# Kernel optimization log

Hardware: AMD Instinct MI355X
Metric: run time of the kernel (lower is better)

Reference implementation:

```python
import jax, jax.numpy as jnp
import numpy as np

B, S, D_MODEL, N_HEAD, D_HEAD = 4, 2048, 512, 8, 64


def setup_inputs() -> dict:
    key = jax.random.key(0)
    ks = jax.random.split(key, 12)
    s = 0.02
    Q = jax.random.normal(ks[0], (B, S, D_MODEL), jnp.float32)
    K = jax.random.normal(ks[1], (B, S, D_MODEL), jnp.float32)
    V = jax.random.normal(ks[2], (B, S, D_MODEL), jnp.float32)
    # causal 0/1 mask, 1 = masked-out (scores get -1e9*mask)
    causal = jnp.triu(jnp.ones((S, S), jnp.float32), k=1)
    attn_mask = jnp.broadcast_to(causal, (B, S, S))
    Wq = jax.random.normal(ks[3], (D_MODEL, N_HEAD * D_HEAD), jnp.float32) * s
    bq = jnp.zeros((N_HEAD * D_HEAD,), jnp.float32)
    Wk = jax.random.normal(ks[4], (D_MODEL, N_HEAD * D_HEAD), jnp.float32) * s
    bk = jnp.zeros((N_HEAD * D_HEAD,), jnp.float32)
    Wv = jax.random.normal(ks[5], (D_MODEL, N_HEAD * D_HEAD), jnp.float32) * s
    bv = jnp.zeros((N_HEAD * D_HEAD,), jnp.float32)
    Wo = jax.random.normal(ks[6], (N_HEAD * D_HEAD, D_MODEL), jnp.float32) * s
    bo = jnp.zeros((D_MODEL,), jnp.float32)
    return {"Q": Q, "K": K, "V": V, "attn_mask": attn_mask,
            "Wq": Wq, "bq": bq, "Wk": Wk, "bk": bk,
            "Wv": Wv, "bv": bv, "Wo": Wo, "bo": bo}


def reference(Q, K, V, attn_mask, Wq, bq, Wk, bk, Wv, bv, Wo, bo):
    # project and split heads: [B,S,D] -> [B,H,S,Dh]
    def heads(x, W, b):
        return (x @ W + b).reshape(B, S, N_HEAD, D_HEAD).transpose(0, 2, 1, 3)

    Qh, Kh, Vh = heads(Q, Wq, bq), heads(K, Wk, bk), heads(V, Wv, bv)
    scale = jnp.sqrt(jnp.asarray(D_HEAD, jnp.float32))
    scores = jnp.einsum('bhqd,bhkd->bhqk', Qh, Kh) / scale  # [B,H,S,S]
    scores = scores - 1e9 * attn_mask[:, None, :, :]
    probs = jax.nn.softmax(scores, axis=-1)
    out = jnp.einsum('bhqk,bhkd->bhqd', probs, Vh)
    out = out.transpose(0, 2, 1, 3).reshape(B, S, N_HEAD * D_HEAD)
    return out @ Wo + bo
```

## Files before the change

kernel.cpp:

```cpp
#include <hip/hip_runtime.h>
#include <hip/hip_bf16.h>
#include <cstdint>
#include <cstddef>

#define B_DIM   4
#define S_DIM   2048
#define DMODEL  512
#define N_HEAD  8
#define D_HEAD  64
#define M_TOT   (B_DIM*S_DIM)

typedef __attribute__((ext_vector_type(8))) short bf16x8;
typedef __attribute__((ext_vector_type(4))) float f32x4;
typedef __attribute__((ext_vector_type(4))) unsigned short us4;
typedef __attribute__((ext_vector_type(2))) unsigned int u32x2;
typedef __attribute__((ext_vector_type(4))) unsigned int u32x4;

static __device__ __forceinline__ unsigned short f2bf(float x) {
  unsigned int u = __float_as_uint(x);
  unsigned int r = (u + 0x7fffu + ((u >> 16) & 1u)) >> 16;
  return (unsigned short)r;
}

static __device__ __forceinline__ unsigned int cvtpk(float lo, float hi) {
  unsigned int r;
  asm("v_cvt_pk_bf16_f32 %0, %1, %2" : "=v"(r) : "v"(lo), "v"(hi));
  return r;
}

static __device__ __forceinline__ void gl2lds16(const unsigned short* g, unsigned short* l) {
  __builtin_amdgcn_global_load_lds(
      (const __attribute__((address_space(1))) void*)g,
      (__attribute__((address_space(3))) void*)l, 16, 0, 0);
}
static __device__ __forceinline__ void gl2lds16f(const float* g, float* l) {
  __builtin_amdgcn_global_load_lds(
      (const __attribute__((address_space(1))) void*)g,
      (__attribute__((address_space(3))) void*)l, 16, 0, 0);
}

__global__ __launch_bounds__(256) void wprep_kernel(
    const float* __restrict__ wq, const float* __restrict__ wk,
    const float* __restrict__ wv, const float* __restrict__ wo,
    unsigned short* __restrict__ out)
{
  __shared__ float T[64][65];
  const int w = blockIdx.x >> 6, tile = blockIdx.x & 63;
  const float* W = (w==0)? wq : (w==1)? wk : (w==2)? wv : wo;
  unsigned short* O = out + (size_t)w*DMODEL*DMODEL;
  const int k0 = (tile>>3)*64, n0 = (tile&7)*64;
  const int tid = threadIdx.x;
  #pragma unroll
  for (int i=0;i<16;i++){
    int flat = tid + i*256; int r = flat>>6, c = flat&63;
    T[r][c] = W[(size_t)(k0+r)*DMODEL + n0 + c];
  }
  __syncthreads();
  #pragma unroll
  for (int i=0;i<16;i++){
    int flat = tid + i*256; int r = flat>>6, c = flat&63;
    O[(size_t)(n0+r)*DMODEL + k0 + c] = f2bf(T[c][r]);
  }
}

__global__ __launch_bounds__(256) void proj_kernel(
    const float* __restrict__ Qf, const float* __restrict__ Kf,
    const float* __restrict__ Vf, const unsigned short* __restrict__ Wtr,
    const float* __restrict__ bq, const float* __restrict__ bk, const float* __restrict__ bv,
    unsigned short* __restrict__ Qh, unsigned short* __restrict__ Kh, unsigned short* __restrict__ Vht)
{
  __shared__ __align__(16) float          Af[2][128*32];
  __shared__ __align__(16) unsigned short Bt[2][128*32];
  const int mode = blockIdx.z;
  const float* A = (mode==0)? Qf : (mode==1)? Kf : Vf;
  const unsigned short* Wt = Wtr + (size_t)mode*DMODEL*DMODEL;
  const float* bias = (mode==0)? bq : (mode==1)? bk : bv;
  const int tid = threadIdx.x, wave = tid>>6, lane = tid&63;
  const int g = lane>>4, ln = lane&15;
  const int mB = blockIdx.y*128, nB = blockIdx.x*128;
  const int mw = (wave>>1)*64,  nw = (wave&1)*64;
  const int lrowA = lane>>3, suF = ((lane&7) ^ (lane>>3))*4;
  const int srow = lane>>2, scolE = (lane&3)*8;
  const int cA = 2*wave, cB = 2*wave+1;

  #define STG(buf, k0_)                                                        \
    do {                                                                       \
      _Pragma("unroll")                                                        \
      for (int q=0;q<4;q++)                                                    \
        gl2lds16f(A + (size_t)(mB + (wave*4+q)*8 + lrowA)*DMODEL + (k0_) + suF,\
                  &Af[buf][(wave*4+q)*256]);                                   \
      gl2lds16(Wt + (size_t)(nB + cA*16 + srow)*DMODEL + (k0_) + scolE, &Bt[buf][cA*512]); \
      gl2lds16(Wt + (size_t)(nB + cB*16 + srow)*DMODEL + (k0_) + scolE, &Bt[buf][cB*512]); \
    } while (0)

  f32x4 acc[4][4];
  #pragma unroll
  for (int i=0;i<4;i++)
    #pragma unroll
    for (int jj=0;jj<4;jj++) acc[i][jj]=(f32x4){0.f,0.f,0.f,0.f};

  STG(0, 0);
  __syncthreads();
  for (int s=0; s<16; ++s){
    const int cur = s&1;
    if (s+1 < 16) STG(cur^1, (s+1)*32);
    bf16x8 a[4], bb[4];
    #pragma unroll
    for (int rf=0;rf<4;rf++){
      const int row = mw + rf*16 + ln;
      const int u0 = (2*g)   ^ (ln&7);
      const int u1 = (2*g+1) ^ (ln&7);
      f32x4 x0 = *(const f32x4*)&Af[cur][row*32 + u0*4];
      f32x4 x1 = *(const f32x4*)&Af[cur][row*32 + u1*4];
      union { u32x4 u; bf16x8 b; } t;
      t.u[0] = cvtpk(x0[0], x0[1]);
      t.u[1] = cvtpk(x0[2], x0[3]);
      t.u[2] = cvtpk(x1[0], x1[1]);
      t.u[3] = cvtpk(x1[2], x1[3]);
      a[rf] = t.b;
    }
    #pragma unroll
    for (int cf=0;cf<4;cf++) bb[cf] = *(const bf16x8*)(&Bt[cur][(nw + cf*16 + ln)*32 + g*8]);
    __builtin_amdgcn_s_setprio(1);
    #pragma unroll
    for (int rf=0;rf<4;rf++)
      #pragma unroll
      for (int cf=0;cf<4;cf++)
        acc[rf][cf] = __builtin_amdgcn_mfma_f32_16x16x32_bf16(a[rf], bb[cf], acc[rf][cf], 0,0,0);
    __builtin_amdgcn_s_setprio(0);
    __syncthreads();
  }
  #undef STG

  const int m0 = mB + mw, n0 = nB + nw;
  float bvv[4];
  #pragma unroll
  for (int cf=0;cf<4;cf++) bvv[cf] = bias[n0 + cf*16 + ln];
  const float QSC = 0.18033688011112042f;

  if (mode <= 1) {
    unsigned short* O = (mode==0)? Qh : Kh;
    const float sc = (mode==0)? QSC : 1.0f;
    #pragma unroll
    for (int rf=0;rf<4;rf++){
      int m = m0 + rf*16 + 4*g;
      int b2 = m >> 11, sdx = m & (S_DIM-1);
      #pragma unroll
      for (int cf=0;cf<4;cf++){
        int n = n0 + cf*16 + ln;
        int h = n >> 6, d = n & 63;
        size_t base = ((size_t)(b2*N_HEAD + h)*S_DIM + sdx)*D_HEAD + d;
        #pragma unroll
        for (int r=0;r<4;r++)
          O[base + (size_t)r*D_HEAD] = f2bf((acc[rf][cf][r] + bvv[cf]) * sc);
      }
    }
  } else {
    #pragma unroll
    for (int rf=0;rf<4;rf++){
      int m = m0 + rf*16 + 4*g;
      int b2 = m >> 11, sdx = m & (S_DIM-1);
      #pragma unroll
      for (int cf=0;cf<4;cf++){
        int n = n0 + cf*16 + ln;
        int h = n >> 6, d = n & 63;
        us4 pk;
        #pragma unroll
        for (int r=0;r<4;r++) pk[r] = f2bf(acc[rf][cf][r] + bvv[cf]);
        *(us4*)&Vht[((size_t)(b2*N_HEAD + h)*D_HEAD + d)*S_DIM + sdx] = pk;
      }
    }
  }
}

__global__ __launch_bounds__(512,4) void attn_kernel(
    const unsigned short* __restrict__ Qh, const unsigned short* __restrict__ Kh,
    const unsigned short* __restrict__ Vht, unsigned short* __restrict__ AO)
{
  __shared__ __align__(16) unsigned short Kt[2][64*64];
  __shared__ __align__(16) unsigned short Vt[2][64*64];
  __shared__ __align__(16) unsigned short Plds[8][16][72];

  const int tid = threadIdx.x, wave = tid>>6, lane = tid&63;
  const int g = lane>>4, ln = lane&15;
  const int j = blockIdx.x;
  const int xcd = j & 7, rest = j >> 3;
  const int bh = xcd*4 + (rest & 3);
  const int t  = 15 - (rest >> 2);
  const int qrow0 = t*128 + wave*16;
  const int q_i = qrow0 + ln;
  const int nit = 2*t + 2;
  const int b = bh >> 3, h = bh & 7;

  const unsigned short* Qp = Qh  + (size_t)bh*S_DIM*D_HEAD;
  const unsigned short* Kp = Kh  + (size_t)bh*S_DIM*D_HEAD;
  const unsigned short* Vp = Vht + (size_t)bh*D_HEAD*S_DIM;

  const int lrow = lane >> 3;
  const int scol = (((lane & 7) ^ lrow) << 3);
  const int swz  = (lane & 7) << 3;
  const unsigned short* kg = Kp + (size_t)(wave*8 + lrow)*64 + scol;
  const unsigned short* vg = Vp + (size_t)(wave*8 + lrow)*S_DIM + scol;

  #define STG_KV(buf, k0_)                                   \
    do {                                                     \
      gl2lds16(kg + (size_t)(k0_)*64, &Kt[buf][wave*512]);   \
      gl2lds16(vg + (k0_),            &Vt[buf][wave*512]);   \
    } while (0)

  bf16x8 qf0 = *(const bf16x8*)(Qp + (size_t)(qrow0+ln)*D_HEAD + 8*g);
  bf16x8 qf1 = *(const bf16x8*)(Qp + (size_t)(qrow0+ln)*D_HEAD + 32 + 8*g);

  f32x4 o[4];
  #pragma unroll
  for (int cc=0;cc<4;cc++) o[cc] = (f32x4){0.f,0.f,0.f,0.f};
  float lsum = 0.f;

  STG_KV(0, 0);
  __syncthreads();

  for (int it = 0; it < nit; ++it) {
    const int cur = it & 1;
    if (it + 1 < nit) STG_KV(cur^1, (it+1)*64);
    const unsigned short* Kc = Kt[cur];
    const unsigned short* Vc = Vt[cur];

    f32x4 s[4];
    __builtin_amdgcn_s_setprio(1);
    #pragma unroll
    for (int i=0;i<4;i++){
      const int r = i*16 + ln;
      bf16x8 ka0 = *(const bf16x8*)(Kc + r*64 + ((g*8) ^ swz));
      bf16x8 ka1 = *(const bf16x8*)(Kc + r*64 + ((32 + g*8) ^ swz));
      f32x4 z = (f32x4){0.f,0.f,0.f,0.f};
      z = __builtin_amdgcn_mfma_f32_16x16x32_bf16(ka0, qf0, z, 0,0,0);
      z = __builtin_amdgcn_mfma_f32_16x16x32_bf16(ka1, qf1, z, 0,0,0);
      s[i] = z;
    }
    __builtin_amdgcn_s_setprio(0);
    const int k0 = it*64;
    if (k0 + 63 > q_i - ln) {
      #pragma unroll
      for (int i=0;i<4;i++)
        #pragma unroll
        for (int r=0;r<4;r++)
          if (k0 + i*16 + 4*g + r > q_i) s[i][r] = -1e30f;
    }
    float p[4][4];
    #pragma unroll
    for (int i=0;i<4;i++)
      #pragma unroll
      for (int r=0;r<4;r++){
        float e = __builtin_amdgcn_exp2f(s[i][r]);
        p[i][r] = e; lsum += e;
      }
    #pragma unroll
    for (int i=0;i<4;i++){
      u32x2 pk2;
      pk2[0] = cvtpk(p[i][0], p[i][1]);
      pk2[1] = cvtpk(p[i][2], p[i][3]);
      *(u32x2*)&Plds[wave][ln][i*16 + 4*g] = pk2;
    }
    bf16x8 pa0 = *(const bf16x8*)&Plds[wave][ln][8*g];
    bf16x8 pa1 = *(const bf16x8*)&Plds[wave][ln][32 + 8*g];
    __builtin_amdgcn_s_setprio(1);
    #pragma unroll
    for (int cc=0;cc<4;cc++){
      const int r = cc*16 + ln;
      bf16x8 vb0 = *(const bf16x8*)(Vc + r*64 + ((g*8) ^ swz));
      bf16x8 vb1 = *(const bf16x8*)(Vc + r*64 + ((32 + g*8) ^ swz));
      o[cc] = __builtin_amdgcn_mfma_f32_16x16x32_bf16(pa0, vb0, o[cc], 0,0,0);
      o[cc] = __builtin_amdgcn_mfma_f32_16x16x32_bf16(pa1, vb1, o[cc], 0,0,0);
    }
    __builtin_amdgcn_s_setprio(0);
    __syncthreads();
  }
  #undef STG_KV

  float lt = lsum;
  lt += __shfl_xor(lt, 16, 64);
  lt += __shfl_xor(lt, 32, 64);
  #pragma unroll
  for (int r=0;r<4;r++){
    float lq  = __shfl(lt, 4*g + r, 64);
    float inv = 1.0f / lq;
    int srow2 = qrow0 + 4*g + r;
    size_t base = ((size_t)b*S_DIM + srow2)*DMODEL + h*D_HEAD;
    #pragma unroll
    for (int cc=0;cc<4;cc++)
      AO[base + cc*16 + ln] = f2bf(o[cc][r]*inv);
  }
}

__global__ __launch_bounds__(256) void outproj_kernel(
    const unsigned short* __restrict__ AO, const unsigned short* __restrict__ Wt,
    const float* __restrict__ bo, float* __restrict__ Out)
{
  __shared__ __align__(16) unsigned short At[2][128*32];
  __shared__ __align__(16) unsigned short Bt[2][128*32];
  const int tid = threadIdx.x, wave = tid>>6, lane = tid&63;
  const int g = lane>>4, ln = lane&15;
  const int mB = blockIdx.y*128, nB = blockIdx.x*128;
  const int mw = (wave>>1)*64,  nw = (wave&1)*64;
  const int srow = lane>>2, scolE = (lane&3)*8;
  const int cA = 2*wave, cB = 2*wave+1;

  #define STG_G(buf, k0_)                                                      \
    do {                                                                       \
      gl2lds16(AO + (size_t)(mB + cA*16 + srow)*DMODEL + (k0_) + scolE, &At[buf][cA*512]); \
      gl2lds16(AO + (size_t)(mB + cB*16 + srow)*DMODEL + (k0_) + scolE, &At[buf][cB*512]); \
      gl2lds16(Wt + (size_t)(nB + cA*16 + srow)*DMODEL + (k0_) + scolE, &Bt[buf][cA*512]); \
      gl2lds16(Wt + (size_t)(nB + cB*16 + srow)*DMODEL + (k0_) + scolE, &Bt[buf][cB*512]); \
    } while (0)

  f32x4 acc[4][4];
  #pragma unroll
  for (int i=0;i<4;i++)
    #pragma unroll
    for (int jj=0;jj<4;jj++) acc[i][jj]=(f32x4){0.f,0.f,0.f,0.f};

  STG_G(0, 0);
  __syncthreads();
  for (int s=0; s<16; ++s){
    const int cur = s&1;
    if (s+1 < 16) STG_G(cur^1, (s+1)*32);
    bf16x8 a[4], bb[4];
    #pragma unroll
    for (int rf=0;rf<4;rf++) a[rf]  = *(const bf16x8*)(&At[cur][(mw + rf*16 + ln)*32 + g*8]);
    #pragma unroll
    for (int cf=0;cf<4;cf++) bb[cf] = *(const bf16x8*)(&Bt[cur][(nw + cf*16 + ln)*32 + g*8]);
    __builtin_amdgcn_s_setprio(1);
    #pragma unroll
    for (int rf=0;rf<4;rf++)
      #pragma unroll
      for (int cf=0;cf<4;cf++)
        acc[rf][cf] = __builtin_amdgcn_mfma_f32_16x16x32_bf16(a[rf], bb[cf], acc[rf][cf], 0,0,0);
    __builtin_amdgcn_s_setprio(0);
    __syncthreads();
  }
  #undef STG_G

  const int m0 = mB + mw, n0 = nB + nw;
  float bvv[4];
  #pragma unroll
  for (int cf=0;cf<4;cf++) bvv[cf] = bo[n0 + cf*16 + ln];
  #pragma unroll
  for (int rf=0;rf<4;rf++){
    #pragma unroll
    for (int cf=0;cf<4;cf++){
      int n = n0 + cf*16 + ln;
      #pragma unroll
      for (int r=0;r<4;r++){
        int m = m0 + rf*16 + 4*g + r;
        Out[(size_t)m*DMODEL + n] = acc[rf][cf][r] + bvv[cf];
      }
    }
  }
}

extern "C" void kernel_launch(void* const* d_in, const int* in_sizes, int n_in,
                              void* d_out, int out_size, void* d_ws, size_t ws_size,
                              hipStream_t stream)
{
  const float* Q  = (const float*)d_in[0];
  const float* K  = (const float*)d_in[1];
  const float* V  = (const float*)d_in[2];
  const float* Wq = (const float*)d_in[4];
  const float* bq = (const float*)d_in[5];
  const float* Wk = (const float*)d_in[6];
  const float* bk = (const float*)d_in[7];
  const float* Wv = (const float*)d_in[8];
  const float* bv = (const float*)d_in[9];
  const float* Wo = (const float*)d_in[10];
  const float* bo = (const float*)d_in[11];

  unsigned short* ws = (unsigned short*)d_ws;
  const size_t TEN = (size_t)M_TOT * DMODEL;
  unsigned short* Wtr = ws;
  unsigned short* Qh  = Wtr + (size_t)4*DMODEL*DMODEL;
  unsigned short* Kh  = Qh + TEN;
  unsigned short* Vht = Kh + TEN;
  unsigned short* AO  = Vht + TEN;

  wprep_kernel  <<<dim3(256),    256, 0, stream>>>(Wq,Wk,Wv,Wo,Wtr);
  proj_kernel   <<<dim3(4,64,3), 256, 0, stream>>>(Q,K,V,Wtr,bq,bk,bv,Qh,Kh,Vht);
  attn_kernel   <<<dim3(512),    512, 0, stream>>>(Qh,Kh,Vht,AO);
  outproj_kernel<<<dim3(4,64),   256, 0, stream>>>(AO, Wtr + (size_t)3*DMODEL*DMODEL, bo, (float*)d_out);
}
```

Measured before the change: 226.9 us.

## Fuse all four stages into one cooperative persistent kernel with grid syncs

Replaces the four separate launches (weight prep, QKV projection, attention, output projection) with a single cooperative kernel of 256 blocks of 512 threads. Grid-wide syncs separate the stages, and one 64 KB LDS arena is reused by every stage. Projection tiles grow to 128x256 per block, and each attention block handles two causal q-tiles (t and 15-t) to balance work. The aim is to remove launch gaps and tail effects between kernels. The cost is fewer blocks in flight (256 versus 512 or 768 before), idle blocks during the projection and output stages, and grid.sync overhead.

Measured after the change: 571.5 us. 2.52x slower.

```diff
diff --git a/kernel.cpp b/kernel.cpp
--- a/kernel.cpp
+++ b/kernel.cpp
@@ -1,7 +1,10 @@
 #include <hip/hip_runtime.h>
+#include <hip/hip_cooperative_groups.h>
 #include <hip/hip_bf16.h>
 #include <cstdint>
 #include <cstddef>
+
+namespace cg = cooperative_groups;
 
 #define B_DIM   4
 #define S_DIM   2048
@@ -21,13 +24,11 @@
   unsigned int r = (u + 0x7fffu + ((u >> 16) & 1u)) >> 16;
   return (unsigned short)r;
 }
-
 static __device__ __forceinline__ unsigned int cvtpk(float lo, float hi) {
   unsigned int r;
   asm("v_cvt_pk_bf16_f32 %0, %1, %2" : "=v"(r) : "v"(lo), "v"(hi));
   return r;
 }
-
 static __device__ __forceinline__ void gl2lds16(const unsigned short* g, unsigned short* l) {
   __builtin_amdgcn_global_load_lds(
       (const __attribute__((address_space(1))) void*)g,
@@ -39,320 +40,320 @@
       (__attribute__((address_space(3))) void*)l, 16, 0, 0);
 }
 
-__global__ __launch_bounds__(256) void wprep_kernel(
-    const float* __restrict__ wq, const float* __restrict__ wk,
-    const float* __restrict__ wv, const float* __restrict__ wo,
-    unsigned short* __restrict__ out)
+__global__ __launch_bounds__(512,2) void fused_kernel(
+    const float* __restrict__ Q, const float* __restrict__ K, const float* __restrict__ V,
+    const float* __restrict__ Wq, const float* __restrict__ bq,
+    const float* __restrict__ Wk, const float* __restrict__ bk,
+    const float* __restrict__ Wv, const float* __restrict__ bv,
+    const float* __restrict__ Wo, const float* __restrict__ bo,
+    unsigned short* __restrict__ Wtr, unsigned short* __restrict__ Qh,
+    unsigned short* __restrict__ Kh, unsigned short* __restrict__ Vht,
+    unsigned short* __restrict__ AO, float* __restrict__ Out)
 {
-  __shared__ float T[64][65];
-  const int w = blockIdx.x >> 6, tile = blockIdx.x & 63;
-  const float* W = (w==0)? wq : (w==1)? wk : (w==2)? wv : wo;
-  unsigned short* O = out + (size_t)w*DMODEL*DMODEL;
-  const int k0 = (tile>>3)*64, n0 = (tile&7)*64;
-  const int tid = threadIdx.x;
-  #pragma unroll
-  for (int i=0;i<16;i++){
-    int flat = tid + i*256; int r = flat>>6, c = flat&63;
-    T[r][c] = W[(size_t)(k0+r)*DMODEL + n0 + c];
-  }
-  __syncthreads();
-  #pragma unroll
-  for (int i=0;i<16;i++){
-    int flat = tid + i*256; int r = flat>>6, c = flat&63;
-    O[(size_t)(n0+r)*DMODEL + k0 + c] = f2bf(T[c][r]);
-  }
-}
-
-__global__ __launch_bounds__(256) void proj_kernel(
-    const float* __restrict__ Qf, const float* __restrict__ Kf,
-    const float* __restrict__ Vf, const unsigned short* __restrict__ Wtr,
-    const float* __restrict__ bq, const float* __restrict__ bk, const float* __restrict__ bv,
-    unsigned short* __restrict__ Qh, unsigned short* __restrict__ Kh, unsigned short* __restrict__ Vht)
-{
-  __shared__ __align__(16) float          Af[2][128*32];
-  __shared__ __align__(16) unsigned short Bt[2][128*32];
-  const int mode = blockIdx.z;
-  const float* A = (mode==0)? Qf : (mode==1)? Kf : Vf;
-  const unsigned short* Wt = Wtr + (size_t)mode*DMODEL*DMODEL;
-  const float* bias = (mode==0)? bq : (mode==1)? bk : bv;
+  __shared__ __align__(16) char arena[65536];
+  cg::grid_group grid = cg::this_grid();
   const int tid = threadIdx.x, wave = tid>>6, lane = tid&63;
   const int g = lane>>4, ln = lane&15;
-  const int mB = blockIdx.y*128, nB = blockIdx.x*128;
-  const int mw = (wave>>1)*64,  nw = (wave&1)*64;
-  const int lrowA = lane>>3, suF = ((lane&7) ^ (lane>>3))*4;
-  const int srow = lane>>2, scolE = (lane&3)*8;
-  const int cA = 2*wave, cB = 2*wave+1;
-
-  #define STG(buf, k0_)                                                        \
-    do {                                                                       \
-      _Pragma("unroll")                                                        \
-      for (int q=0;q<4;q++)                                                    \
-        gl2lds16f(A + (size_t)(mB + (wave*4+q)*8 + lrowA)*DMODEL + (k0_) + suF,\
-                  &Af[buf][(wave*4+q)*256]);                                   \
-      gl2lds16(Wt + (size_t)(nB + cA*16 + srow)*DMODEL + (k0_) + scolE, &Bt[buf][cA*512]); \
-      gl2lds16(Wt + (size_t)(nB + cB*16 + srow)*DMODEL + (k0_) + scolE, &Bt[buf][cB*512]); \
-    } while (0)
-
-  f32x4 acc[4][4];
-  #pragma unroll
-  for (int i=0;i<4;i++)
-    #pragma unroll
-    for (int jj=0;jj<4;jj++) acc[i][jj]=(f32x4){0.f,0.f,0.f,0.f};
-
-  STG(0, 0);
-  __syncthreads();
-  for (int s=0; s<16; ++s){
-    const int cur = s&1;
-    if (s+1 < 16) STG(cur^1, (s+1)*32);
-    bf16x8 a[4], bb[4];
+  const int blk = blockIdx.x;
+
+  {
+    float (*T)[65] = (float(*)[65])arena;
+    const int w = blk >> 6, t64 = blk & 63;
+    const float* W = (w==0)? Wq : (w==1)? Wk : (w==2)? Wv : Wo;
+    unsigned short* O = Wtr + (size_t)w*DMODEL*DMODEL;
+    const int k0 = (t64>>3)*64, n0 = (t64&7)*64;
+    #pragma unroll
+    for (int i=0;i<8;i++){
+      int f = tid + i*512; int r = f>>6, c = f&63;
+      T[r][c] = W[(size_t)(k0+r)*DMODEL + n0 + c];
+    }
+    __syncthreads();
+    #pragma unroll
+    for (int i=0;i<8;i++){
+      int f = tid + i*512; int r = f>>6, c = f&63;
+      O[(size_t)(n0+r)*DMODEL + k0 + c] = f2bf(T[c][r]);
+    }
+  }
+  __threadfence(); grid.sync(); __threadfence();
+
+  if (blk < 192) {
+    float          (*Af)[4096] = (float(*)[4096])arena;
+    unsigned short (*Bt)[8192] = (unsigned short(*)[8192])(arena+32768);
+    const int mode = blk / 64, mBp = blk % 64;
+    const float* A = (mode==0)? Q : (mode==1)? K : V;
+    const unsigned short* Wt = Wtr + (size_t)mode*DMODEL*DMODEL;
+    const float* bias = (mode==0)? bq : (mode==1)? bk : bv;
+    const int mw = (wave>>2)*64, nw = (wave&3)*64;
+    const int lrowA = lane>>3, suF = ((lane&7)^(lane>>3))*4;
+    const int srow = lane>>2, scolE = (lane&3)*8;
+    const int ca0 = wave*2, ca1 = wave*2+1;
+    const float* Abase = A + (size_t)mBp*128*DMODEL;
+    const float QSC = 0.18033688011112042f;
+
+    for (int h2 = 0; h2 < 2; ++h2) {
+      const unsigned short* Wh = Wt + (size_t)h2*256*DMODEL;
+      #define STG1(buf, k0_)                                                         \
+        do {                                                                         \
+          gl2lds16f(Abase + (size_t)(ca0*8+lrowA)*DMODEL + (k0_) + suF, &Af[buf][ca0*256]); \
+          gl2lds16f(Abase + (size_t)(ca1*8+lrowA)*DMODEL + (k0_) + suF, &Af[buf][ca1*256]); \
+          gl2lds16(Wh + (size_t)(ca0*16+srow)*DMODEL + (k0_) + scolE, &Bt[buf][ca0*512]);  \
+          gl2lds16(Wh + (size_t)(ca1*16+srow)*DMODEL + (k0_) + scolE, &Bt[buf][ca1*512]);  \
+        } while (0)
+
+      f32x4 acc[4][4];
+      #pragma unroll
+      for (int i=0;i<4;i++)
+        #pragma unroll
+        for (int jj=0;jj<4;jj++) acc[i][jj]=(f32x4){0.f,0.f,0.f,0.f};
+
+      STG1(0, 0);
+      __syncthreads();
+      for (int s=0; s<16; ++s){
+        const int cur = s&1;
+        if (s+1 < 16) STG1(cur^1, (s+1)*32);
+        bf16x8 a[4], bb[4];
+        #pragma unroll
+        for (int rf=0;rf<4;rf++){
+          const int row = mw + rf*16 + ln;
+          const int u0 = (2*g)   ^ (ln&7);
+          const int u1 = (2*g+1) ^ (ln&7);
+          f32x4 x0 = *(const f32x4*)&Af[cur][row*32 + u0*4];
+          f32x4 x1 = *(const f32x4*)&Af[cur][row*32 + u1*4];
+          union { u32x4 u; bf16x8 b; } t;
+          t.u[0] = cvtpk(x0[0], x0[1]);
+          t.u[1] = cvtpk(x0[2], x0[3]);
+          t.u[2] = cvtpk(x1[0], x1[1]);
+          t.u[3] = cvtpk(x1[2], x1[3]);
+          a[rf] = t.b;
+        }
+        #pragma unroll
+        for (int cf=0;cf<4;cf++) bb[cf] = *(const bf16x8*)(&Bt[cur][(nw + cf*16 + ln)*32 + g*8]);
+        __builtin_amdgcn_s_setprio(1);
+        #pragma unroll
+        for (int rf=0;rf<4;rf++)
+          #pragma unroll
+          for (int cf=0;cf<4;cf++)
+            acc[rf][cf] = __builtin_amdgcn_mfma_f32_16x16x32_bf16(a[rf], bb[cf], acc[rf][cf], 0,0,0);
+        __builtin_amdgcn_s_setprio(0);
+        __syncthreads();
+      }
+      #undef STG1
+
+      float bvv[4];
+      #pragma unroll
+      for (int cf=0;cf<4;cf++) bvv[cf] = bias[h2*256 + nw + cf*16 + ln];
+
+      if (mode <= 1) {
+        unsigned short* O = (mode==0)? Qh : Kh;
+        const float sc = (mode==0)? QSC : 1.0f;
+        #pragma unroll
+        for (int rf=0;rf<4;rf++){
+          int m = mBp*128 + mw + rf*16 + 4*g;
+          int b2 = m >> 11, sdx = m & (S_DIM-1);
+          #pragma unroll
+          for (int cf=0;cf<4;cf++){
+            int n = h2*256 + nw + cf*16 + ln;
+            int h = n >> 6, d = n & 63;
+            size_t base = ((size_t)(b2*N_HEAD + h)*S_DIM + sdx)*D_HEAD + d;
+            #pragma unroll
+            for (int r=0;r<4;r++)
+              O[base + (size_t)r*D_HEAD] = f2bf((acc[rf][cf][r] + bvv[cf]) * sc);
+          }
+        }
+      } else {
+        #pragma unroll
+        for (int rf=0;rf<4;rf++){
+          int m = mBp*128 + mw + rf*16 + 4*g;
+          int b2 = m >> 11, sdx = m & (S_DIM-1);
+          #pragma unroll
+          for (int cf=0;cf<4;cf++){
+            int n = h2*256 + nw + cf*16 + ln;
+            int h = n >> 6, d = n & 63;
+            us4 pk;
+            #pragma unroll
+            for (int r=0;r<4;r++) pk[r] = f2bf(acc[rf][cf][r] + bvv[cf]);
+            *(us4*)&Vht[((size_t)(b2*N_HEAD + h)*D_HEAD + d)*S_DIM + sdx] = pk;
+          }
+        }
+      }
+      __syncthreads();
+    }
+  }
+  __threadfence(); grid.sync(); __threadfence();
+
+  {
+    unsigned short (*Kt)[4096]    = (unsigned short(*)[4096])arena;
+    unsigned short (*Vt)[4096]    = (unsigned short(*)[4096])(arena+16384);
+    unsigned short (*Plds)[16][72]= (unsigned short(*)[16][72])(arena+32768);
+    const int xcd = blk & 7, m3 = (blk>>3)&3, p = blk>>5;
+    const int bh = xcd*4 + m3;
+    const int b = bh >> 3, h = bh & 7;
+    const unsigned short* Qp = Qh  + (size_t)bh*S_DIM*D_HEAD;
+    const unsigned short* Kp = Kh  + (size_t)bh*S_DIM*D_HEAD;
+    const unsigned short* Vp = Vht + (size_t)bh*D_HEAD*S_DIM;
+    const int lrow = lane >> 3;
+    const int scol = (((lane & 7) ^ lrow) << 3);
+    const int swz  = (lane & 7) << 3;
+    const unsigned short* kg = Kp + (size_t)(wave*8 + lrow)*64 + scol;
+    const unsigned short* vg = Vp + (size_t)(wave*8 + lrow)*S_DIM + scol;
+
+    #define STG_KV(buf, k0_)                                   \
+      do {                                                     \
+        gl2lds16(kg + (size_t)(k0_)*64, &Kt[buf][wave*512]);   \
+        gl2lds16(vg + (k0_),            &Vt[buf][wave*512]);   \
+      } while (0)
+
+    #pragma unroll 1
+    for (int sel = 0; sel < 2; ++sel) {
+      const int t = sel ? p : (15 - p);
+      const int qrow0 = t*128 + wave*16;
+      const int q_i = qrow0 + ln;
+      const int nit = 2*t + 2;
+
+      bf16x8 qf0 = *(const bf16x8*)(Qp + (size_t)(qrow0+ln)*D_HEAD + 8*g);
+      bf16x8 qf1 = *(const bf16x8*)(Qp + (size_t)(qrow0+ln)*D_HEAD + 32 + 8*g);
+
+      f32x4 o[4];
+      #pragma unroll
+      for (int cc=0;cc<4;cc++) o[cc] = (f32x4){0.f,0.f,0.f,0.f};
+      float lsum = 0.f;
+
+      STG_KV(0, 0);
+      __syncthreads();
+
+      for (int it = 0; it < nit; ++it) {
+        const int cur = it & 1;
+        if (it + 1 < nit) STG_KV(cur^1, (it+1)*64);
+        const unsigned short* Kc = Kt[cur];
+        const unsigned short* Vc = Vt[cur];
+
+        f32x4 s[4];
+        __builtin_amdgcn_s_setprio(1);
+        #pragma unroll
+        for (int i=0;i<4;i++){
+          const int r = i*16 + ln;
+          bf16x8 ka0 = *(const bf16x8*)(Kc + r*64 + ((g*8) ^ swz));
+          bf16x8 ka1 = *(const bf16x8*)(Kc + r*64 + ((32 + g*8) ^ swz));
+          f32x4 z = (f32x4){0.f,0.f,0.f,0.f};
+          z = __builtin_amdgcn_mfma_f32_16x16x32_bf16(ka0, qf0, z, 0,0,0);
+          z = __builtin_amdgcn_mfma_f32_16x16x32_bf16(ka1, qf1, z, 0,0,0);
+          s[i] = z;
+        }
+        __builtin_amdgcn_s_setprio(0);
+        const int k0 = it*64;
+        if (k0 + 63 > q_i - ln) {
+          #pragma unroll
+          for (int i=0;i<4;i++)
+            #pragma unroll
+            for (int r=0;r<4;r++)
+              if (k0 + i*16 + 4*g + r > q_i) s[i][r] = -1e30f;
+        }
+        float pp[4][4];
+        #pragma unroll
+        for (int i=0;i<4;i++)
+          #pragma unroll
+          for (int r=0;r<4;r++){
+            float e = __builtin_amdgcn_exp2f(s[i][r]);
+            pp[i][r] = e; lsum += e;
+          }
+        #pragma unroll
+        for (int i=0;i<4;i++){
+          u32x2 pk2;
+          pk2[0] = cvtpk(pp[i][0], pp[i][1]);
+          pk2[1] = cvtpk(pp[i][2], pp[i][3]);
+          *(u32x2*)&Plds[wave][ln][i*16 + 4*g] = pk2;
+        }
+        bf16x8 pa0 = *(const bf16x8*)&Plds[wave][ln][8*g];
+        bf16x8 pa1 = *(const bf16x8*)&Plds[wave][ln][32 + 8*g];
+        __builtin_amdgcn_s_setprio(1);
+        #pragma unroll
+        for (int cc=0;cc<4;cc++){
+          const int r = cc*16 + ln;
+          bf16x8 vb0 = *(const bf16x8*)(Vc + r*64 + ((g*8) ^ swz));
+          bf16x8 vb1 = *(const bf16x8*)(Vc + r*64 + ((32 + g*8) ^ swz));
+          o[cc] = __builtin_amdgcn_mfma_f32_16x16x32_bf16(pa0, vb0, o[cc], 0,0,0);
+          o[cc] = __builtin_amdgcn_mfma_f32_16x16x32_bf16(pa1, vb1, o[cc], 0,0,0);
+        }
+        __builtin_amdgcn_s_setprio(0);
+        __syncthreads();
+      }
+
+      float lt = lsum;
+      lt += __shfl_xor(lt, 16, 64);
+      lt += __shfl_xor(lt, 32, 64);
+      #pragma unroll
+      for (int r=0;r<4;r++){
+        float lq  = __shfl(lt, 4*g + r, 64);
+        float inv = 1.0f / lq;
+        int srow2 = qrow0 + 4*g + r;
+        size_t base = ((size_t)b*S_DIM + srow2)*DMODEL + h*D_HEAD;
+        #pragma unroll
+        for (int cc=0;cc<4;cc++)
+          AO[base + cc*16 + ln] = f2bf(o[cc][r]*inv);
+      }
+      __syncthreads();
+    }
+    #undef STG_KV
+  }
+  __threadfence(); grid.sync(); __threadfence();
+
+  if (blk < 128) {
+    unsigned short (*At)[4096] = (unsigned short(*)[4096])arena;
+    unsigned short (*Bt)[8192] = (unsigned short(*)[8192])(arena+16384);
+    const int mBp = blk >> 1, h2 = blk & 1;
+    const unsigned short* Wt = Wtr + (size_t)3*DMODEL*DMODEL + (size_t)h2*256*DMODEL;
+    const unsigned short* Ab = AO + (size_t)mBp*128*DMODEL;
+    const int mw = (wave>>2)*64, nw = (wave&3)*64;
+    const int srow = lane>>2, scolE = (lane&3)*8;
+    const int ca0 = wave*2, ca1 = wave*2+1;
+
+    #define STG3(buf, k0_)                                                            \
+      do {                                                                            \
+        gl2lds16(Ab + (size_t)(wave*16+srow)*DMODEL + (k0_) + scolE, &At[buf][wave*512]); \
+        gl2lds16(Wt + (size_t)(ca0*16+srow)*DMODEL + (k0_) + scolE, &Bt[buf][ca0*512]);   \
+        gl2lds16(Wt + (size_t)(ca1*16+srow)*DMODEL + (k0_) + scolE, &Bt[buf][ca1*512]);   \
+      } while (0)
+
+    f32x4 acc[4][4];
+    #pragma unroll
+    for (int i=0;i<4;i++)
+      #pragma unroll
+      for (int jj=0;jj<4;jj++) acc[i][jj]=(f32x4){0.f,0.f,0.f,0.f};
+
+    STG3(0, 0);
+    __syncthreads();
+    for (int s=0; s<16; ++s){
+      const int cur = s&1;
+      if (s+1 < 16) STG3(cur^1, (s+1)*32);
+      bf16x8 a[4], bb[4];
+      #pragma unroll
+      for (int rf=0;rf<4;rf++) a[rf]  = *(const bf16x8*)(&At[cur][(mw + rf*16 + ln)*32 + g*8]);
+      #pragma unroll
+      for (int cf=0;cf<4;cf++) bb[cf] = *(const bf16x8*)(&Bt[cur][(nw + cf*16 + ln)*32 + g*8]);
+      __builtin_amdgcn_s_setprio(1);
+      #pragma unroll
+      for (int rf=0;rf<4;rf++)
+        #pragma unroll
+        for (int cf=0;cf<4;cf++)
+          acc[rf][cf] = __builtin_amdgcn_mfma_f32_16x16x32_bf16(a[rf], bb[cf], acc[rf][cf], 0,0,0);
+      __builtin_amdgcn_s_setprio(0);
+      __syncthreads();
+    }
+    #undef STG3
+
+    float bvv[4];
+    #pragma unroll
+    for (int cf=0;cf<4;cf++) bvv[cf] = bo[h2*256 + nw + cf*16 + ln];
     #pragma unroll
     for (int rf=0;rf<4;rf++){
-      const int row = mw + rf*16 + ln;
-      const int u0 = (2*g)   ^ (ln&7);
-      const int u1 = (2*g+1) ^ (ln&7);
-      f32x4 x0 = *(const f32x4*)&Af[cur][row*32 + u0*4];
-      f32x4 x1 = *(const f32x4*)&Af[cur][row*32 + u1*4];
-      union { u32x4 u; bf16x8 b; } t;
-      t.u[0] = cvtpk(x0[0], x0[1]);
-      t.u[1] = cvtpk(x0[2], x0[3]);
-      t.u[2] = cvtpk(x1[0], x1[1]);
-      t.u[3] = cvtpk(x1[2], x1[3]);
-      a[rf] = t.b;
-    }
-    #pragma unroll
-    for (int cf=0;cf<4;cf++) bb[cf] = *(const bf16x8*)(&Bt[cur][(nw + cf*16 + ln)*32 + g*8]);
-    __builtin_amdgcn_s_setprio(1);
-    #pragma unroll
-    for (int rf=0;rf<4;rf++)
-      #pragma unroll
-      for (int cf=0;cf<4;cf++)
-        acc[rf][cf] = __builtin_amdgcn_mfma_f32_16x16x32_bf16(a[rf], bb[cf], acc[rf][cf], 0,0,0);
-    __builtin_amdgcn_s_setprio(0);
-    __syncthreads();
-  }
-  #undef STG
-
-  const int m0 = mB + mw, n0 = nB + nw;
-  float bvv[4];
-  #pragma unroll
-  for (int cf=0;cf<4;cf++) bvv[cf] = bias[n0 + cf*16 + ln];
-  const float QSC = 0.18033688011112042f;
-
-  if (mode <= 1) {
-    unsigned short* O = (mode==0)? Qh : Kh;
-    const float sc = (mode==0)? QSC : 1.0f;
-    #pragma unroll
-    for (int rf=0;rf<4;rf++){
-      int m = m0 + rf*16 + 4*g;
-      int b2 = m >> 11, sdx = m & (S_DIM-1);
       #pragma unroll
       for (int cf=0;cf<4;cf++){
-        int n = n0 + cf*16 + ln;
-        int h = n >> 6, d = n & 63;
-        size_t base = ((size_t)(b2*N_HEAD + h)*S_DIM + sdx)*D_HEAD + d;
-        #pragma unroll
-        for (int r=0;r<4;r++)
-          O[base + (size_t)r*D_HEAD] = f2bf((acc[rf][cf][r] + bvv[cf]) * sc);
-      }
-    }
-  } else {
-    #pragma unroll
-    for (int rf=0;rf<4;rf++){
-      int m = m0 + rf*16 + 4*g;
-      int b2 = m >> 11, sdx = m & (S_DIM-1);
-      #pragma unroll
-      for (int cf=0;cf<4;cf++){
-        int n = n0 + cf*16 + ln;
-        int h = n >> 6, d = n & 63;
-        us4 pk;
-        #pragma unroll
-        for (int r=0;r<4;r++) pk[r] = f2bf(acc[rf][cf][r] + bvv[cf]);
-        *(us4*)&Vht[((size_t)(b2*N_HEAD + h)*D_HEAD + d)*S_DIM + sdx] = pk;
-      }
-    }
-  }
-}
-
-__global__ __launch_bounds__(512,4) void attn_kernel(
-    const unsigned short* __restrict__ Qh, const unsigned short* __restrict__ Kh,
-    const unsigned short* __restrict__ Vht, unsigned short* __restrict__ AO)
-{
-  __shared__ __align__(16) unsigned short Kt[2][64*64];
-  __shared__ __align__(16) unsigned short Vt[2][64*64];
-  __shared__ __align__(16) unsigned short Plds[8][16][72];
-
-  const int tid = threadIdx.x, wave = tid>>6, lane = tid&63;
-  const int g = lane>>4, ln = lane&15;
-  const int j = blockIdx.x;
-  const int xcd = j & 7, rest = j >> 3;
-  const int bh = xcd*4 + (rest & 3);
-  const int t  = 15 - (rest >> 2);
-  const int qrow0 = t*128 + wave*16;
-  const int q_i = qrow0 + ln;
-  const int nit = 2*t + 2;
-  const int b = bh >> 3, h = bh & 7;
-
-  const unsigned short* Qp = Qh  + (size_t)bh*S_DIM*D_HEAD;
-  const unsigned short* Kp = Kh  + (size_t)bh*S_DIM*D_HEAD;
-  const unsigned short* Vp = Vht + (size_t)bh*D_HEAD*S_DIM;
-
-  const int lrow = lane >> 3;
-  const int scol = (((lane & 7) ^ lrow) << 3);
-  const int swz  = (lane & 7) << 3;
-  const unsigned short* kg = Kp + (size_t)(wave*8 + lrow)*64 + scol;
-  const unsigned short* vg = Vp + (size_t)(wave*8 + lrow)*S_DIM + scol;
-
-  #define STG_KV(buf, k0_)                                   \
-    do {                                                     \
-      gl2lds16(kg + (size_t)(k0_)*64, &Kt[buf][wave*512]);   \
-      gl2lds16(vg + (k0_),            &Vt[buf][wave*512]);   \
-    } while (0)
-
-  bf16x8 qf0 = *(const bf16x8*)(Qp + (size_t)(qrow0+ln)*D_HEAD + 8*g);
-  bf16x8 qf1 = *(const bf16x8*)(Qp + (size_t)(qrow0+ln)*D_HEAD + 32 + 8*g);
-
-  f32x4 o[4];
-  #pragma unroll
-  for (int cc=0;cc<4;cc++) o[cc] = (f32x4){0.f,0.f,0.f,0.f};
-  float lsum = 0.f;
-
-  STG_KV(0, 0);
-  __syncthreads();
-
-  for (int it = 0; it < nit; ++it) {
-    const int cur = it & 1;
-    if (it + 1 < nit) STG_KV(cur^1, (it+1)*64);
-    const unsigned short* Kc = Kt[cur];
-    const unsigned short* Vc = Vt[cur];
-
-    f32x4 s[4];
-    __builtin_amdgcn_s_setprio(1);
-    #pragma unroll
-    for (int i=0;i<4;i++){
-      const int r = i*16 + ln;
-      bf16x8 ka0 = *(const bf16x8*)(Kc + r*64 + ((g*8) ^ swz));
-      bf16x8 ka1 = *(const bf16x8*)(Kc + r*64 + ((32 + g*8) ^ swz));
-      f32x4 z = (f32x4){0.f,0.f,0.f,0.f};
-      z = __builtin_amdgcn_mfma_f32_16x16x32_bf16(ka0, qf0, z, 0,0,0);
-      z = __builtin_amdgcn_mfma_f32_16x16x32_bf16(ka1, qf1, z, 0,0,0);
-      s[i] = z;
-    }
-    __builtin_amdgcn_s_setprio(0);
-    const int k0 = it*64;
-    if (k0 + 63 > q_i - ln) {
-      #pragma unroll
-      for (int i=0;i<4;i++)
-        #pragma unroll
-        for (int r=0;r<4;r++)
-          if (k0 + i*16 + 4*g + r > q_i) s[i][r] = -1e30f;
-    }
-    float p[4][4];
-    #pragma unroll
-    for (int i=0;i<4;i++)
-      #pragma unroll
-      for (int r=0;r<4;r++){
-        float e = __builtin_amdgcn_exp2f(s[i][r]);
-        p[i][r] = e; lsum += e;
-      }
-    #pragma unroll
-    for (int i=0;i<4;i++){
-      u32x2 pk2;
-      pk2[0] = cvtpk(p[i][0], p[i][1]);
-      pk2[1] = cvtpk(p[i][2], p[i][3]);
-      *(u32x2*)&Plds[wave][ln][i*16 + 4*g] = pk2;
-    }
-    bf16x8 pa0 = *(const bf16x8*)&Plds[wave][ln][8*g];
-    bf16x8 pa1 = *(const bf16x8*)&Plds[wave][ln][32 + 8*g];
-    __builtin_amdgcn_s_setprio(1);
-    #pragma unroll
-    for (int cc=0;cc<4;cc++){
-      const int r = cc*16 + ln;
-      bf16x8 vb0 = *(const bf16x8*)(Vc + r*64 + ((g*8) ^ swz));
-      bf16x8 vb1 = *(const bf16x8*)(Vc + r*64 + ((32 + g*8) ^ swz));
-      o[cc] = __builtin_amdgcn_mfma_f32_16x16x32_bf16(pa0, vb0, o[cc], 0,0,0);
-      o[cc] = __builtin_amdgcn_mfma_f32_16x16x32_bf16(pa1, vb1, o[cc], 0,0,0);
-    }
-    __builtin_amdgcn_s_setprio(0);
-    __syncthreads();
-  }
-  #undef STG_KV
-
-  float lt = lsum;
-  lt += __shfl_xor(lt, 16, 64);
-  lt += __shfl_xor(lt, 32, 64);
-  #pragma unroll
-  for (int r=0;r<4;r++){
-    float lq  = __shfl(lt, 4*g + r, 64);
-    float inv = 1.0f / lq;
-    int srow2 = qrow0 + 4*g + r;
-    size_t base = ((size_t)b*S_DIM + srow2)*DMODEL + h*D_HEAD;
-    #pragma unroll
-    for (int cc=0;cc<4;cc++)
-      AO[base + cc*16 + ln] = f2bf(o[cc][r]*inv);
-  }
-}
-
-__global__ __launch_bounds__(256) void outproj_kernel(
-    const unsigned short* __restrict__ AO, const unsigned short* __restrict__ Wt,
-    const float* __restrict__ bo, float* __restrict__ Out)
-{
-  __shared__ __align__(16) unsigned short At[2][128*32];
-  __shared__ __align__(16) unsigned short Bt[2][128*32];
-  const int tid = threadIdx.x, wave = tid>>6, lane = tid&63;
-  const int g = lane>>4, ln = lane&15;
-  const int mB = blockIdx.y*128, nB = blockIdx.x*128;
-  const int mw = (wave>>1)*64,  nw = (wave&1)*64;
-  const int srow = lane>>2, scolE = (lane&3)*8;
-  const int cA = 2*wave, cB = 2*wave+1;
-
-  #define STG_G(buf, k0_)                                                      \
-    do {                                                                       \
-      gl2lds16(AO + (size_t)(mB + cA*16 + srow)*DMODEL + (k0_) + scolE, &At[buf][cA*512]); \
-      gl2lds16(AO + (size_t)(mB + cB*16 + srow)*DMODEL + (k0_) + scolE, &At[buf][cB*512]); \
-      gl2lds16(Wt + (size_t)(nB + cA*16 + srow)*DMODEL + (k0_) + scolE, &Bt[buf][cA*512]); \
-      gl2lds16(Wt + (size_t)(nB + cB*16 + srow)*DMODEL + (k0_) + scolE, &Bt[buf][cB*512]); \
-    } while (0)
-
-  f32x4 acc[4][4];
-  #pragma unroll
-  for (int i=0;i<4;i++)
-    #pragma unroll
-    for (int jj=0;jj<4;jj++) acc[i][jj]=(f32x4){0.f,0.f,0.f,0.f};
-
-  STG_G(0, 0);
-  __syncthreads();
-  for (int s=0; s<16; ++s){
-    const int cur = s&1;
-    if (s+1 < 16) STG_G(cur^1, (s+1)*32);
-    bf16x8 a[4], bb[4];
-    #pragma unroll
-    for (int rf=0;rf<4;rf++) a[rf]  = *(const bf16x8*)(&At[cur][(mw + rf*16 + ln)*32 + g*8]);
-    #pragma unroll
-    for (int cf=0;cf<4;cf++) bb[cf] = *(const bf16x8*)(&Bt[cur][(nw + cf*16 + ln)*32 + g*8]);
-    __builtin_amdgcn_s_setprio(1);
-    #pragma unroll
-    for (int rf=0;rf<4;rf++)
-      #pragma unroll
-      for (int cf=0;cf<4;cf++)
-        acc[rf][cf] = __builtin_amdgcn_mfma_f32_16x16x32_bf16(a[rf], bb[cf], acc[rf][cf], 0,0,0);
-    __builtin_amdgcn_s_setprio(0);
-    __syncthreads();
-  }
-  #undef STG_G
-
-  const int m0 = mB + mw, n0 = nB + nw;
-  float bvv[4];
-  #pragma unroll
-  for (int cf=0;cf<4;cf++) bvv[cf] = bo[n0 + cf*16 + ln];
-  #pragma unroll
-  for (int rf=0;rf<4;rf++){
-    #pragma unroll
-    for (int cf=0;cf<4;cf++){
-      int n = n0 + cf*16 + ln;
-      #pragma unroll
-      for (int r=0;r<4;r++){
-        int m = m0 + rf*16 + 4*g + r;
-        Out[(size_t)m*DMODEL + n] = acc[rf][cf][r] + bvv[cf];
+        int n = h2*256 + nw + cf*16 + ln;
+        #pragma unroll
+        for (int r=0;r<4;r++){
+          int m = mBp*128 + mw + rf*16 + 4*g + r;
+          Out[(size_t)m*DMODEL + n] = acc[rf][cf][r] + bvv[cf];
+        }
       }
     }
   }
@@ -381,9 +382,13 @@
   unsigned short* Kh  = Qh + TEN;
   unsigned short* Vht = Kh + TEN;
   unsigned short* AO  = Vht + TEN;
-
-  wprep_kernel  <<<dim3(256),    256, 0, stream>>>(Wq,Wk,Wv,Wo,Wtr);
-  proj_kernel   <<<dim3(4,64,3), 256, 0, stream>>>(Q,K,V,Wtr,bq,bk,bv,Qh,Kh,Vht);
-  attn_kernel   <<<dim3(512),    512, 0, stream>>>(Qh,Kh,Vht,AO);
-  outproj_kernel<<<dim3(4,64),   256, 0, stream>>>(AO, Wtr + (size_t)3*DMODEL*DMODEL, bo, (float*)d_out);
-}
+  float* Outp = (float*)d_out;
+
+  void* args[] = { (void*)&Q, (void*)&K, (void*)&V,
+                   (void*)&Wq, (void*)&bq, (void*)&Wk, (void*)&bk,
+                   (void*)&Wv, (void*)&bv, (void*)&Wo, (void*)&bo,
+                   (void*)&Wtr, (void*)&Qh, (void*)&Kh, (void*)&Vht,
+                   (void*)&AO, (void*)&Outp };
+  hipLaunchCooperativeKernel((void*)fused_kernel, dim3(256), dim3(512),
+                             args, 0, stream);
+}
```
